# Kernel optimization log

Hardware: AMD Instinct MI355X
Metric: run time of the kernel (lower is better)

## Reference

```python
import jax, jax.numpy as jnp
import numpy as np

B, C, K, L = 2, 64, 256, 128
H = 8
DH = C // H
PROJ = 64
DADP = 10
FFT = 8
NG = 4
EPS = 1e-5
SCALE = float(1.0 / np.sqrt(DH))


def group_norm(x, g, b):
    # x: (B, C, N); GroupNorm(4, C)
    bb, cc, nn = x.shape
    xg = x.reshape(bb, NG, cc // NG, nn)
    mu = jnp.mean(xg, axis=(2, 3), keepdims=True)
    var = jnp.var(xg, axis=(2, 3), keepdims=True)
    xn = ((xg - mu) * jax.lax.rsqrt(var + EPS)).reshape(bb, cc, nn)
    return xn * g[None, :, None] + b[None, :, None]


def layer_norm(x, g, b):
    mu = jnp.mean(x, axis=-1, keepdims=True)
    var = jnp.var(x, axis=-1, keepdims=True)
    return (x - mu) * jax.lax.rsqrt(var + EPS) * g + b


def setup_inputs() -> dict:
    key = jax.random.key(0)
    ks = jax.random.split(key, 24)
    it = iter(ks)

    def nrm(shape, scale=0.05):
        return jax.random.normal(next(it), shape, dtype=jnp.float32) * scale

    z = lambda *s: jnp.zeros(s, jnp.float32)
    o = lambda *s: jnp.ones(s, jnp.float32)
    inp = dict(
        y=jax.random.normal(next(it), (B, C, K * L), dtype=jnp.float32),
        a1=jax.nn.softmax(jax.random.normal(next(it), (K, K), dtype=jnp.float32), axis=1),
        a2=jax.nn.softmax(jax.random.normal(next(it), (K, K), dtype=jnp.float32), axis=1),
        nodevec1=nrm((K, DADP), 0.3), nodevec2=nrm((DADP, K), 0.3),
        gcn_w=nrm((C, 7 * C)), gcn_b=z(C),
        s_wq=nrm((C, C)), s_wk=nrm((C, C)), s_wv=nrm((C, C)),
        s_pk=nrm((K, PROJ), float(1.0 / np.sqrt(PROJ))),
        s_pv=nrm((K, PROJ), float(1.0 / np.sqrt(PROJ))),
        s_wo=nrm((C, C)), s_bo=z(C),
        t_wq=nrm((C, C)), t_wk=nrm((C, C)), t_wv=nrm((C, C)),
        t_bq=z(C), t_bk=z(C), t_bv=z(C),
        t_wo=nrm((C, C)), t_bo=z(C),
        t_l1w=nrm((C, FFT)), t_l1b=z(FFT), t_l2w=nrm((FFT, C)), t_l2b=z(C),
        t_ln1g=o(C), t_ln1b=z(C), t_ln2g=o(C), t_ln2b=z(C),
        gn_local_g=o(C), gn_local_b=z(C),
        gn_s_g=o(C), gn_s_b=z(C),
        gn_t_g=o(C), gn_t_b=z(C),
        ff1_w=nrm((C, 2 * C)), ff1_b=z(2 * C),
        ff2_w=nrm((2 * C, C)), ff2_b=z(C),
        gn2_g=o(C), gn2_b=z(C),
        base_B=B, base_K=K, base_L=L,
    )
    return inp


def reference(y, a1, a2, nodevec1, nodevec2, gcn_w, gcn_b,
              s_wq, s_wk, s_wv, s_pk, s_pv, s_wo, s_bo,
              t_wq, t_wk, t_wv, t_bq, t_bk, t_bv, t_wo, t_bo,
              t_l1w, t_l1b, t_l2w, t_l2b, t_ln1g, t_ln1b, t_ln2g, t_ln2b,
              gn_local_g, gn_local_b, gn_s_g, gn_s_b, gn_t_g, gn_t_b,
              ff1_w, ff1_b, ff2_w, ff2_b, gn2_g, gn2_b,
              base_B, base_K, base_L):
    Bv, Kv, Lv = int(base_B), int(base_K), int(base_L)
    y4 = y.reshape(Bv, C, Kv, Lv)

    # ---- AdaptiveGCN: order-2 conv over [a1, a2, adaptive adj] + self ----
    x = y4.transpose(0, 3, 1, 2)  # (B, L, C, K)
    adp = jax.nn.softmax(jax.nn.relu(nodevec1 @ nodevec2), axis=1)  # (K, K)
    outs = [x]
    for a in (a1, a2, adp):
        x1 = jnp.einsum('blcv,wv->blcw', x, a)
        x2 = jnp.einsum('blcv,wv->blcw', x1, a)
        outs += [x1, x2]
    cat = jnp.concatenate(outs, axis=2)  # (B, L, 7C, K)
    g = jnp.einsum('blik,oi->blok', cat, gcn_w) + gcn_b[None, None, :, None]
    y_local = g.transpose(0, 2, 3, 1).reshape(Bv, C, Kv * Lv)
    y_local = group_norm(y + y_local, gn_local_g, gn_local_b)

    # ---- Linformer-style spatial attention over K ----
    xs = y4.transpose(0, 3, 2, 1).reshape(Bv * Lv, Kv, C)  # (B*L, K, C)
    q = (xs @ s_wq).reshape(-1, Kv, H, DH).transpose(0, 2, 1, 3)
    kp = jnp.einsum('bnd,nk->bkd', xs @ s_wk, s_pk).reshape(-1, PROJ, H, DH).transpose(0, 2, 1, 3)
    vp = jnp.einsum('bnd,nk->bkd', xs @ s_wv, s_pv).reshape(-1, PROJ, H, DH).transpose(0, 2, 1, 3)
    attn = jax.nn.softmax(jnp.einsum('bhnd,bhkd->bhnk', q, kp) * SCALE, axis=-1)
    o = jnp.einsum('bhnk,bhkd->bhnd', attn, vp).transpose(0, 2, 1, 3).reshape(-1, Kv, C)
    o = o @ s_wo + s_bo
    y_s = o.transpose(0, 2, 1).reshape(Bv, Lv, C, Kv).transpose(0, 2, 3, 1).reshape(Bv, C, Kv * Lv)
    y_s = group_norm(y + y_s, gn_s_g, gn_s_b)

    # ---- temporal transformer encoder layer over L ----
    xt = y4.transpose(0, 2, 3, 1).reshape(Bv * Kv, Lv, C)  # (B*K, L, C)
    tq = (xt @ t_wq + t_bq).reshape(-1, Lv, H, DH).transpose(0, 2, 1, 3)
    tk = (xt @ t_wk + t_bk).reshape(-1, Lv, H, DH).transpose(0, 2, 1, 3)
    tv = (xt @ t_wv + t_bv).reshape(-1, Lv, H, DH).transpose(0, 2, 1, 3)
    ta = jax.nn.softmax(jnp.einsum('bhnd,bhkd->bhnk', tq, tk) * SCALE, axis=-1)
    to = jnp.einsum('bhnk,bhkd->bhnd', ta, tv).transpose(0, 2, 1, 3).reshape(-1, Lv, C)
    to = to @ t_wo + t_bo
    src = layer_norm(xt + to, t_ln1g, t_ln1b)
    ff = jax.nn.gelu(src @ t_l1w + t_l1b, approximate=False) @ t_l2w + t_l2b
    src = layer_norm(src + ff, t_ln2g, t_ln2b)
    y_t = src.transpose(0, 2, 1).reshape(Bv, Kv, C, Lv).transpose(0, 2, 1, 3).reshape(Bv, C, Kv * Lv)
    y_t = group_norm(y + y_t, gn_t_g, gn_t_b)

    # ---- fuse + channel FFN + final norm ----
    y_in2 = y_local + y_s + y_t
    h = jax.nn.relu(y_in2.transpose(0, 2, 1) @ ff1_w + ff1_b)
    h = (h @ ff2_w + ff2_b).transpose(0, 2, 1)
    return group_norm(h + y_in2, gn2_g, gn2_b)
```

## Files before the change

### kernel.cpp

```cpp
#include <hip/hip_runtime.h>
#include <math.h>

constexpr int CC = 64, KK = 256, LL = 128;
constexpr int NN = KK * LL;
constexpr int PR = 64;
constexpr int CPG = 16;
constexpr float EPSV = 1e-5f;
constexpr float SCL = 0.35355339059327373f;

typedef __attribute__((ext_vector_type(8))) short short8;
typedef __attribute__((ext_vector_type(4))) float f32x4;

__device__ __forceinline__ unsigned short f2bf(float x) {
  union { float f; unsigned int u; } v; v.f = x;
  unsigned int r = (v.u + 0x7FFFu + ((v.u >> 16) & 1u)) >> 16;
  return (unsigned short)r;
}
__device__ __forceinline__ float bf2f(unsigned short x) {
  union { unsigned int u; float f; } v; v.u = ((unsigned int)x) << 16;
  return v.f;
}

__global__ __launch_bounds__(256) void k_adp(const float* __restrict__ nv1,
                                             const float* __restrict__ nv2,
// ... 291 lines not shown
      short8 b1 = *(const short8*)(wqT + (size_t)(ct * 16 + lr) * 64 + 32 + g * 8);
      acc[ct] = __builtin_amdgcn_mfma_f32_16x16x32_bf16(ax0, b0, acc[ct], 0, 0, 0);
      acc[ct] = __builtin_amdgcn_mfma_f32_16x16x32_bf16(ax1, b1, acc[ct], 0, 0, 0);
    }
#pragma unroll
    for (int ct = 0; ct < 4; ++ct)
#pragma unroll
      for (int reg = 0; reg < 4; ++reg)
        qb[(size_t)(r0 + w * 16 + g * 4 + reg) * 64 + ct * 16 + lr] = f2bf(acc[ct][reg]);
  }
  short8 bx0[4], bx1[4];
#pragma unroll
  for (int ct = 0; ct < 4; ++ct) {
    const unsigned short* bP = Xbf + (size_t)(r0 + ct * 16 + lr) * 64 + g * 8;
    bx0[ct] = *(const short8*)bP;
    bx1[ct] = *(const short8*)(bP + 32);
  }
  int bl = r0 >> 8, nb = r0 & 255;
#pragma unroll
  for (int which = 0; which < 2; ++which) {
    const unsigned short* WT = which ? wvT : wkT;
    unsigned short* dstb = which ? xvT : xkT;
    short8 aw0 = *(const short8*)(WT + (size_t)(w * 16 + lr) * 64 + g * 8);
    short8 aw1 = *(const short8*)(WT + (size_t)(w * 16 + lr) * 64 + 32 + g * 8);
    f32x4 acc[4];
#pragma unroll
    for (int ct = 0; ct < 4; ++ct) {
      acc[ct] = f32x4{0.f, 0.f, 0.f, 0.f};
      acc[ct] = __builtin_amdgcn_mfma_f32_16x16x32_bf16(aw0, bx0[ct], acc[ct], 0, 0, 0);
      acc[ct] = __builtin_amdgcn_mfma_f32_16x16x32_bf16(aw1, bx1[ct], acc[ct], 0, 0, 0);
    }
#pragma unroll
    for (int ct = 0; ct < 4; ++ct)
#pragma unroll
      for (int reg = 0; reg < 4; ++reg) {
        int o = w * 16 + g * 4 + reg;
        dstb[(size_t)bl * 16384 + (size_t)o * 256 + nb + ct * 16 + lr] = f2bf(acc[ct][reg]);
      }
  }
}

__global__ __launch_bounds__(256) void k_qkvt_M(const unsigned short* __restrict__ Xbf,
                                                const unsigned short* __restrict__ wqT,
                                                const unsigned short* __restrict__ wkT,
                                                const unsigned short* __restrict__ wvT,
                                                const float* __restrict__ bq, const float* __restrict__ bk_,
                                                const float* __restrict__ bv,
                                                unsigned short* __restrict__ qb,
                                                unsigned short* __restrict__ kb,
                                                unsigned short* __restrict__ vt) {
  int r0 = blockIdx.x * 64;
  int t = threadIdx.x, w = t >> 6, lane = t & 63;
  int lr = lane & 15, g = lane >> 4;
  const unsigned short* aP = Xbf + (size_t)(r0 + w * 16 + lr) * 64 + g * 8;
  short8 ax0 = *(const short8*)aP;
  short8 ax1 = *(const short8*)(aP + 32);
#pragma unroll
  for (int which = 0; which < 2; ++which) {
    const unsigned short* WT = which ? wkT : wqT;
    const float* bias = which ? bk_ : bq;
    unsigned short* dstb = which ? kb : qb;
    f32x4 acc[4];
#pragma unroll
    for (int ct = 0; ct < 4; ++ct) {
      acc[ct] = f32x4{0.f, 0.f, 0.f, 0.f};
      short8 b0 = *(const short8*)(WT + (size_t)(ct * 16 + lr) * 64 + g * 8);
      short8 b1 = *(const short8*)(WT + (size_t)(ct * 16 + lr) * 64 + 32 + g * 8);
      acc[ct] = __builtin_amdgcn_mfma_f32_16x16x32_bf16(ax0, b0, acc[ct], 0, 0, 0);
      acc[ct] = __builtin_amdgcn_mfma_f32_16x16x32_bf16(ax1, b1, acc[ct], 0, 0, 0);
    }
#pragma unroll
    for (int ct = 0; ct < 4; ++ct) {
      float bvv = bias[ct * 16 + lr];
#pragma unroll
      for (int reg = 0; reg < 4; ++reg)
        dstb[(size_t)(r0 + w * 16 + g * 4 + reg) * 64 + ct * 16 + lr] = f2bf(acc[ct][reg] + bvv);
    }
  }
  short8 bx0[4], bx1[4];
#pragma unroll
  for (int ct = 0; ct < 4; ++ct) {
    const unsigned short* bP = Xbf + (size_t)(r0 + ct * 16 + lr) * 64 + g * 8;
    bx0[ct] = *(const short8*)bP;
    bx1[ct] = *(const short8*)(bP + 32);
  }
  int bkk = r0 >> 7, lbase = r0 & 127;
  short8 aw0 = *(const short8*)(wvT + (size_t)(w * 16 + lr) * 64 + g * 8);
  short8 aw1 = *(const short8*)(wvT + (size_t)(w * 16 + lr) * 64 + 32 + g * 8);
  f32x4 acc[4];
#pragma unroll
  for (int ct = 0; ct < 4; ++ct) {
    acc[ct] = f32x4{0.f, 0.f, 0.f, 0.f};
    acc[ct] = __builtin_amdgcn_mfma_f32_16x16x32_bf16(aw0, bx0[ct], acc[ct], 0, 0, 0);
    acc[ct] = __builtin_amdgcn_mfma_f32_16x16x32_bf16(aw1, bx1[ct], acc[ct], 0, 0, 0);
  }
#pragma unroll
  for (int ct = 0; ct < 4; ++ct)
#pragma unroll
    for (int reg = 0; reg < 4; ++reg) {
      int o = w * 16 + g * 4 + reg;
      vt[(size_t)bkk * 8192 + (size_t)o * 128 + lbase + ct * 16 + lr] = f2bf(acc[ct][reg] + bv[o]);
    }
}

__global__ __launch_bounds__(256) void k_sprojM(const unsigned short* __restrict__ XkT,
                                                const unsigned short* __restrict__ XvT,
                                                const unsigned short* __restrict__ PkT,
                                                const unsigned short* __restrict__ PvT,
                                                unsigned short* __restrict__ kpb,
                                                unsigned short* __restrict__ vptb) {
  int bl = blockIdx.x;
  int which = blockIdx.y;
  int t = threadIdx.x, w = t >> 6, lane = t & 63;
  int lr = lane & 15, g = lane >> 4;
  const unsigned short* Abase = which ? PvT : XkT + (size_t)bl * 16384;
  const unsigned short* Bbase = which ? XvT + (size_t)bl * 16384 : PkT;
  const unsigned short* aP = Abase + (size_t)(w * 16 + lr) * 256 + g * 8;
  f32x4 acc[4];
#pragma unroll
  for (int ct = 0; ct < 4; ++ct) acc[ct] = f32x4{0.f, 0.f, 0.f, 0.f};
  for (int k0 = 0; k0 < 256; k0 += 32) {
    short8 af = *(const short8*)(aP + k0);
#pragma unroll
    for (int ct = 0; ct < 4; ++ct) {
      short8 bf = *(const short8*)(Bbase + (size_t)(ct * 16 + lr) * 256 + k0 + g * 8);
      acc[ct] = __builtin_amdgcn_mfma_f32_16x16x32_bf16(af, bf, acc[ct], 0, 0, 0);
    }
  }
  if (!which) {
    unsigned short* dst = kpb + (size_t)bl * 4096;
#pragma unroll
    for (int ct = 0; ct < 4; ++ct) {
      int p = ct * 16 + lr;
      int c0 = w * 16 + g * 4;
      ushort4 pk;
      pk.x = f2bf(acc[ct][0]); pk.y = f2bf(acc[ct][1]);
      pk.z = f2bf(acc[ct][2]); pk.w = f2bf(acc[ct][3]);
      *(ushort4*)&dst[(size_t)p * 64 + c0] = pk;
    }
  } else {
    unsigned short* dst = vptb + (size_t)bl * 4096;
#pragma unroll
    for (int ct = 0; ct < 4; ++ct) {
      int c = ct * 16 + lr;
      int p0 = w * 16 + g * 4;
      ushort4 pk;
      pk.x = f2bf(acc[ct][0]); pk.y = f2bf(acc[ct][1]);
      pk.z = f2bf(acc[ct][2]); pk.w = f2bf(acc[ct][3]);
      *(ushort4*)&dst[(size_t)c * 64 + p0] = pk;
    }
  }
}

__global__ __launch_bounds__(256) void k_lin64(const unsigned short* __restrict__ in,
                                               const unsigned short* __restrict__ WT,
                                               const float* __restrict__ bias,
                                               float* __restrict__ out) {
  int r0 = blockIdx.x * 64;
  int t = threadIdx.x, w = t >> 6, lane = t & 63;
  int lr = lane & 15, g = lane >> 4;
  const unsigned short* aP = in + (size_t)(r0 + w * 16 + lr) * 64 + g * 8;
  short8 af0 = *(const short8*)aP;
  short8 af1 = *(const short8*)(aP + 32);
  f32x4 acc[4];
#pragma unroll
  for (int ct = 0; ct < 4; ++ct) acc[ct] = f32x4{0.f, 0.f, 0.f, 0.f};
#pragma unroll
  for (int ct = 0; ct < 4; ++ct) {
    short8 b0 = *(const short8*)(WT + (size_t)(ct * 16 + lr) * 64 + g * 8);
    short8 b1 = *(const short8*)(WT + (size_t)(ct * 16 + lr) * 64 + 32 + g * 8);
    acc[ct] = __builtin_amdgcn_mfma_f32_16x16x32_bf16(af0, b0, acc[ct], 0, 0, 0);
    acc[ct] = __builtin_amdgcn_mfma_f32_16x16x32_bf16(af1, b1, acc[ct], 0, 0, 0);
  }
#pragma unroll
  for (int ct = 0; ct < 4; ++ct) {
    int o = ct * 16 + lr;
    float bv = bias[o];
#pragma unroll
    for (int reg = 0; reg < 4; ++reg)
      out[(size_t)(r0 + w * 16 + g * 4 + reg) * 64 + o] = acc[ct][reg] + bv;
  }
}

__global__ __launch_bounds__(256) void k_cffn(const unsigned short* __restrict__ in,
                                              const unsigned short* __restrict__ ff1T,
                                              const unsigned short* __restrict__ ff2T,
                                              const float* __restrict__ b1,
                                              const float* __restrict__ b2,
                                              float* __restrict__ out) {
  __shared__ unsigned short sH[4][16 * 128];
  int r0 = blockIdx.x * 64;
  int t = threadIdx.x, w = t >> 6, lane = t & 63;
  int lr = lane & 15, g = lane >> 4;
  unsigned short* myH = sH[w];
  const unsigned short* aP = in + (size_t)(r0 + w * 16 + lr) * 64 + g * 8;
  short8 af0 = *(const short8*)aP;
  short8 af1 = *(const short8*)(aP + 32);
  f32x4 acc1[8];
#pragma unroll
  for (int ct = 0; ct < 8; ++ct) acc1[ct] = f32x4{0.f, 0.f, 0.f, 0.f};
#pragma unroll
  for (int ct = 0; ct < 8; ++ct) {
    short8 b0 = *(const short8*)(ff1T + (size_t)(ct * 16 + lr) * 64 + g * 8);
    short8 bx = *(const short8*)(ff1T + (size_t)(ct * 16 + lr) * 64 + 32 + g * 8);
    acc1[ct] = __builtin_amdgcn_mfma_f32_16x16x32_bf16(af0, b0, acc1[ct], 0, 0, 0);
    acc1[ct] = __builtin_amdgcn_mfma_f32_16x16x32_bf16(af1, bx, acc1[ct], 0, 0, 0);
  }
#pragma unroll
  for (int ct = 0; ct < 8; ++ct) {
    int o = ct * 16 + lr;
    float bv = b1[o];
#pragma unroll
    for (int reg = 0; reg < 4; ++reg) {
      int m = g * 4 + reg;
      float h = fmaxf(acc1[ct][reg] + bv, 0.f);
      int bo = ((m * 128 + o) * 2) ^ ((m & 7) << 4);
      *(unsigned short*)((char*)myH + bo) = f2bf(h);
    }
  }
  __syncthreads();
  short8 ha[4];
#pragma unroll
  for (int ks = 0; ks < 4; ++ks) {
    int bo = ((lr * 128 + ks * 32 + g * 8) * 2) ^ ((lr & 7) << 4);
    ha[ks] = *(const short8*)((char*)myH + bo);
  }
  f32x4 acc2[4];
#pragma unroll
  for (int ct = 0; ct < 4; ++ct) acc2[ct] = f32x4{0.f, 0.f, 0.f, 0.f};
#pragma unroll
  for (int ct = 0; ct < 4; ++ct)
#pragma unroll
    for (int ks = 0; ks < 4; ++ks) {
      short8 b0 = *(const short8*)(ff2T + (size_t)(ct * 16 + lr) * 128 + ks * 32 + g * 8);
      acc2[ct] = __builtin_amdgcn_mfma_f32_16x16x32_bf16(ha[ks], b0, acc2[ct], 0, 0, 0);
    }
#pragma unroll
  for (int ct = 0; ct < 4; ++ct) {
    int o = ct * 16 + lr;
    float bv = b2[o];
#pragma unroll
    for (int reg = 0; reg < 4; ++reg)
      out[(size_t)(r0 + w * 16 + g * 4 + reg) * 64 + o] = acc2[ct][reg] + bv;
  }
}

__global__ __launch_bounds__(256) void k_tffn(const float* __restrict__ A, const float* __restrict__ Bz,
                                              const float* __restrict__ l1w, const float* __restrict__ l1b,
                                              const float* __restrict__ l2w, const float* __restrict__ l2b,
                                              const float* __restrict__ ln1g, const float* __restrict__ ln1b,
                                              const float* __restrict__ ln2g, const float* __restrict__ ln2b,
                                              float* __restrict__ outp) {
  int r0 = blockIdx.x * 64;
  __shared__ float sSrc[64][65];
  __shared__ float sH[64][8];
  __shared__ float sW1[64][8];
  __shared__ float sW2[8][64];
  int t = threadIdx.x;
  for (int i = t; i < 512; i += 256) { ((float*)sW1)[i] = l1w[i]; ((float*)sW2)[i] = l2w[i]; }
  int c = t & 63, rg = t >> 6;
  float g1 = ln1g[c], be1 = ln1b[c];
  for (int it = 0; it < 16; ++it) {
    int r = it * 4 + rg;
    size_t idx = (size_t)(r0 + r) * 64 + c;
    float x = A[idx] + Bz[idx];
    float s = x, ss = x * x;
#pragma unroll
    for (int off = 32; off; off >>= 1) { s += __shfl_xor(s, off); ss += __shfl_xor(ss, off); }
    float mu = s * (1.f / 64.f);
    float var = ss * (1.f / 64.f) - mu * mu;
    sSrc[r][c] = (x - mu) * rsqrtf(var + EPSV) * g1 + be1;
  }
  __syncthreads();
#pragma unroll
  for (int p = 0; p < 2; ++p) {
    int idx = t + 256 * p;
    int row = idx >> 3, j = idx & 7;
    float acc = l1b[j];
    for (int cc = 0; cc < 64; ++cc) acc += sSrc[row][cc] * sW1[cc][j];
    acc = 0.5f * acc * (1.f + erff(acc * 0.70710678118654752440f));
    sH[row][j] = acc;
  }
  __syncthreads();
  float g2 = ln2g[c], be2 = ln2b[c];
  float l2bc = l2b[c];
  for (int it = 0; it < 16; ++it) {
    int r = it * 4 + rg;
    float o = l2bc;
#pragma unroll
    for (int j = 0; j < 8; ++j) o += sH[r][j] * sW2[j][c];
    float x = sSrc[r][c] + o;
    float s = x, ss = x * x;
#pragma unroll
    for (int off = 32; off; off >>= 1) { s += __shfl_xor(s, off); ss += __shfl_xor(ss, off); }
    float mu = s * (1.f / 64.f);
    float var = ss * (1.f / 64.f) - mu * mu;
    outp[(size_t)(r0 + r) * 64 + c] = (x - mu) * rsqrtf(var + EPSV) * g2 + be2;
  }
}

template <int NKV, int KVSHIFT>
__global__ __launch_bounds__(512) void k_attnH(const unsigned short* __restrict__ Qb,
                                               const unsigned short* __restrict__ Kb,
                                               const unsigned short* __restrict__ VTb,
                                               unsigned short* __restrict__ O) {
  constexpr int NCT = NKV / 16;
  constexpr int NKS = NKV / 32;
  int blk = blockIdx.x;
  const unsigned short* Qp = Qb + (size_t)blk * 128 * 64;
  unsigned short* Op = O + (size_t)blk * 128 * 64;
  const unsigned short* Kp = Kb + (size_t)(blk >> KVSHIFT) * NKV * 64;
  const unsigned short* VTp = VTb + (size_t)(blk >> KVSHIFT) * 64 * NKV;
  int t = threadIdx.x;
  int h = t >> 6, lane = t & 63, lr = lane & 15, g = lane >> 4;
  __shared__ unsigned short sP[8][16 * NKV];
  unsigned short* myP = sP[h];

  short8 kbf[NCT];
#pragma unroll
  for (int ct = 0; ct < NCT; ++ct)
    kbf[ct] = *(const short8*)(Kp + (size_t)(ct * 16 + lr) * 64 + h * 8);

  int vr = h * 8 + lr; if (vr > 63) vr = 63;
  short8 vbf[NKS];
#pragma unroll
  for (int ks = 0; ks < NKS; ++ks)
    vbf[ks] = *(const short8*)(VTp + (size_t)vr * NKV + ks * 32 + g * 8);

  for (int mt = 0; mt < 8; ++mt) {
    short8 qa = short8{0, 0, 0, 0, 0, 0, 0, 0};
    if (g == 0) qa = *(const short8*)(Qp + (size_t)(mt * 16 + lr) * 64 + h * 8);

    f32x4 sacc[NCT];
#pragma unroll
    for (int ct = 0; ct < NCT; ++ct) sacc[ct] = f32x4{0.f, 0.f, 0.f, 0.f};
#pragma unroll
    for (int ct = 0; ct < NCT; ++ct)
      sacc[ct] = __builtin_amdgcn_mfma_f32_16x16x32_bf16(qa, kbf[ct], sacc[ct], 0, 0, 0);

    float inv4[4];
#pragma unroll
    for (int reg = 0; reg < 4; ++reg) {
      float s = 0.f;
#pragma unroll
      for (int ct = 0; ct < NCT; ++ct) {
        float e = __expf(sacc[ct][reg] * SCL);
        sacc[ct][reg] = e;
        s += e;
      }
      s += __shfl_xor(s, 1); s += __shfl_xor(s, 2); s += __shfl_xor(s, 4); s += __shfl_xor(s, 8);
      inv4[reg] = 1.f / s;
    }

#pragma unroll
    for (int ct = 0; ct < NCT; ++ct)
#pragma unroll
      for (int reg = 0; reg < 4; ++reg) {
        int row = g * 4 + reg;
        int bo = ((row * NKV + ct * 16 + lr) * 2) ^ ((row & 7) << 4);
        *(unsigned short*)((char*)myP + bo) = f2bf(sacc[ct][reg]);
      }
    __syncthreads();

    f32x4 oacc = f32x4{0.f, 0.f, 0.f, 0.f};
#pragma unroll
    for (int ks = 0; ks < NKS; ++ks) {
      int bo = ((lr * NKV + ks * 32 + g * 8) * 2) ^ ((lr & 7) << 4);
      short8 pa = *(const short8*)((char*)myP + bo);
      oacc = __builtin_amdgcn_mfma_f32_16x16x32_bf16(pa, vbf[ks], oacc, 0, 0, 0);
    }
    if (lr < 8) {
#pragma unroll
      for (int reg = 0; reg < 4; ++reg) {
        int row = mt * 16 + g * 4 + reg;
        Op[(size_t)row * 64 + h * 8 + lr] = f2bf(oacc[reg] * inv4[reg]);
      }
    }
    __syncthreads();
  }
}

__global__ __launch_bounds__(256) void k_gn_part(const float* __restrict__ p0, const float* __restrict__ p1,
                                                 const float* __restrict__ p2, const float* __restrict__ p3,
                                                 const float* __restrict__ p4,
                                                 float* __restrict__ sumOut,
                                                 float* __restrict__ part) {
  int bg = blockIdx.y, blk = blockIdx.x, t = threadIdx.x;
  size_t start = (size_t)bg * ((size_t)CPG * NN) + (size_t)blk * 8192;
  const float4* q0 = (const float4*)(p0 + start);
  const float4* q1 = p1 ? (const float4*)(p1 + start) : nullptr;
  const float4* q2 = p2 ? (const float4*)(p2 + start) : nullptr;
  const float4* q3 = p3 ? (const float4*)(p3 + start) : nullptr;
  const float4* q4 = p4 ? (const float4*)(p4 + start) : nullptr;
  float4* so = sumOut ? (float4*)(sumOut + start) : nullptr;
  float s = 0.f, ss = 0.f;
  for (int i = t; i < 2048; i += 256) {
    float4 x = q0[i];
    if (q1) { float4 y4 = q1[i]; x.x += y4.x; x.y += y4.y; x.z += y4.z; x.w += y4.w; }
    if (q2) { float4 y4 = q2[i]; x.x += y4.x; x.y += y4.y; x.z += y4.z; x.w += y4.w; }
    if (q3) { float4 y4 = q3[i]; x.x += y4.x; x.y += y4.y; x.z += y4.z; x.w += y4.w; }
    if (q4) { float4 y4 = q4[i]; x.x += y4.x; x.y += y4.y; x.z += y4.z; x.w += y4.w; }
    if (so) so[i] = x;
    s += x.x + x.y + x.z + x.w;
    ss += x.x * x.x + x.y * x.y + x.z * x.z + x.w * x.w;
  }
  __shared__ float rs[256], rq[256];
  rs[t] = s; rq[t] = ss; __syncthreads();
  for (int off = 128; off; off >>= 1) { if (t < off) { rs[t] += rs[t + off]; rq[t] += rq[t + off]; } __syncthreads(); }
  if (t == 0) { part[(bg * 64 + blk) * 2] = rs[0]; part[(bg * 64 + blk) * 2 + 1] = rq[0]; }
}

__global__ __launch_bounds__(256) void k_gn_partB(const float* __restrict__ p0,
                                                  const unsigned short* __restrict__ q1,
                                                  const unsigned short* __restrict__ q2,
                                                  const unsigned short* __restrict__ q3,
                                                  const unsigned short* __restrict__ q4,
                                                  float* __restrict__ sumOut,
                                                  float* __restrict__ part) {
  int bg = blockIdx.y, blk = blockIdx.x, t = threadIdx.x;
  size_t start = (size_t)bg * ((size_t)CPG * NN) + (size_t)blk * 8192;
  const float4* f0 = (const float4*)(p0 + start);
  const ushort4* b1 = (const ushort4*)(q1 + start);
  const ushort4* b2 = (const ushort4*)(q2 + start);
  const ushort4* b3 = (const ushort4*)(q3 + start);
  const ushort4* b4 = (const ushort4*)(q4 + start);
  float4* so = (float4*)(sumOut + start);
  float s = 0.f, ss = 0.f;
  for (int i = t; i < 2048; i += 256) {
    float4 x = f0[i];
    ushort4 u;
    u = b1[i]; x.x += bf2f(u.x); x.y += bf2f(u.y); x.z += bf2f(u.z); x.w += bf2f(u.w);
    u = b2[i]; x.x += bf2f(u.x); x.y += bf2f(u.y); x.z += bf2f(u.z); x.w += bf2f(u.w);
    u = b3[i]; x.x += bf2f(u.x); x.y += bf2f(u.y); x.z += bf2f(u.z); x.w += bf2f(u.w);
    u = b4[i]; x.x += bf2f(u.x); x.y += bf2f(u.y); x.z += bf2f(u.z); x.w += bf2f(u.w);
    so[i] = x;
    s += x.x + x.y + x.z + x.w;
    ss += x.x * x.x + x.y * x.y + x.z * x.z + x.w * x.w;
  }
  __shared__ float rs[256], rq[256];
  rs[t] = s; rq[t] = ss; __syncthreads();
  for (int off = 128; off; off >>= 1) { if (t < off) { rs[t] += rs[t + off]; rq[t] += rq[t + off]; } __syncthreads(); }
  if (t == 0) { part[(bg * 64 + blk) * 2] = rs[0]; part[(bg * 64 + blk) * 2 + 1] = rq[0]; }
}

__global__ __launch_bounds__(256) void k_gn_apply(const float* __restrict__ p0, const float* __restrict__ p1,
                                                  const float* __restrict__ part, const float* __restrict__ g,
                                                  const float* __restrict__ be,
                                                  const float* __restrict__ q0, const float* __restrict__ q1,
                                                  float* __restrict__ out) {
  size_t i4 = (size_t)blockIdx.x * 256 + threadIdx.x;
  size_t i = i4 * 4;
  int chan = (int)(i >> 15) & 63;
  int bg = (int)(i >> 19);
  __shared__ float smu, srr;
  int t = threadIdx.x;
  if (t < 64) {
    float s = part[(bg * 64 + t) * 2], ss = part[(bg * 64 + t) * 2 + 1];
#pragma unroll
    for (int off = 32; off; off >>= 1) { s += __shfl_xor(s, off); ss += __shfl_xor(ss, off); }
    if (t == 0) {
      float inv = 1.f / (float)((size_t)CPG * NN);
      float mu = s * inv;
      float var = ss * inv - mu * mu;
      smu = mu; srr = rsqrtf(var + EPSV);
    }
  }
  __syncthreads();
  float mu = smu, rr = srr;
  float4 x = ((const float4*)p0)[i4];
  if (p1) { float4 y4 = ((const float4*)p1)[i4]; x.x += y4.x; x.y += y4.y; x.z += y4.z; x.w += y4.w; }
  float gc = g[chan], bc = be[chan];
  float4 v;
  v.x = (x.x - mu) * rr * gc + bc;
  v.y = (x.y - mu) * rr * gc + bc;
  v.z = (x.z - mu) * rr * gc + bc;
  v.w = (x.w - mu) * rr * gc + bc;
  if (q0) { float4 y4 = ((const float4*)q0)[i4]; v.x += y4.x; v.y += y4.y; v.z += y4.z; v.w += y4.w; }
  if (q1) { float4 y4 = ((const float4*)q1)[i4]; v.x += y4.x; v.y += y4.y; v.z += y4.z; v.w += y4.w; }
  ((float4*)out)[i4] = v;
}

__global__ __launch_bounds__(256) void k_gn_apply3(const float* __restrict__ SL, const float* __restrict__ SS,
                                                   const float* __restrict__ ST,
                                                   const float* __restrict__ part,
                                                   const float* __restrict__ gl, const float* __restrict__ bl_,
                                                   const float* __restrict__ gs, const float* __restrict__ bs_,
                                                   const float* __restrict__ gt, const float* __restrict__ bt_,
                                                   float* __restrict__ out) {
  size_t i4 = (size_t)blockIdx.x * 256 + threadIdx.x;
  size_t i = i4 * 4;
  int chan = (int)(i >> 15) & 63;
  int bg = (int)(i >> 19);
  __shared__ float smu[3], srr[3];
  int t = threadIdx.x;
  if (t < 192) {
    int which = t >> 6, tt = t & 63;
    const float* pp = part + which * 2048;
    float s = pp[(bg * 64 + tt) * 2], ss = pp[(bg * 64 + tt) * 2 + 1];
#pragma unroll
    for (int off = 32; off; off >>= 1) { s += __shfl_xor(s, off); ss += __shfl_xor(ss, off); }
    if (tt == 0) {
      float inv = 1.f / (float)((size_t)CPG * NN);
      float mu = s * inv;
      float var = ss * inv - mu * mu;
      smu[which] = mu; srr[which] = rsqrtf(var + EPSV);
    }
  }
  __syncthreads();
  float mL = smu[0], rL = srr[0];
  float mS = smu[1], rS = srr[1];
  float mT = smu[2], rT = srr[2];
  float gL = gl[chan] * rL, bL = bl_[chan] - mL * gl[chan] * rL;
  float gS = gs[chan] * rS, bS = bs_[chan] - mS * gs[chan] * rS;
  float gT = gt[chan] * rT, bT = bt_[chan] - mT * gt[chan] * rT;
  float4 xl = ((const float4*)SL)[i4];
  float4 xs = ((const float4*)SS)[i4];
  float4 xt = ((const float4*)ST)[i4];
  float4 v;
  v.x = xl.x * gL + bL + xs.x * gS + bS + xt.x * gT + bT;
  v.y = xl.y * gL + bL + xs.y * gS + bS + xt.y * gT + bT;
  v.z = xl.z * gL + bL + xs.z * gS + bS + xt.z * gT + bT;
  v.w = xl.w * gL + bL + xs.w * gS + bS + xt.w * gT + bT;
  ((float4*)out)[i4] = v;
}

extern "C" void kernel_launch(void* const* d_in, const int* in_sizes, int n_in,
                              void* d_out, int out_size, void* d_ws, size_t ws_size,
                              hipStream_t stream) {
  (void)in_sizes; (void)n_in; (void)out_size; (void)ws_size;
  const float* y     = (const float*)d_in[0];
  const float* a1    = (const float*)d_in[1];
  const float* a2    = (const float*)d_in[2];
  const float* nv1   = (const float*)d_in[3];
  const float* nv2   = (const float*)d_in[4];
  const float* gcn_w = (const float*)d_in[5];
  const float* gcn_b = (const float*)d_in[6];
  const float* s_wq  = (const float*)d_in[7];
  const float* s_wk  = (const float*)d_in[8];
  const float* s_wv  = (const float*)d_in[9];
  const float* s_pk  = (const float*)d_in[10];
  const float* s_pv  = (const float*)d_in[11];
  const float* s_wo  = (const float*)d_in[12];
  const float* s_bo  = (const float*)d_in[13];
  const float* t_wq  = (const float*)d_in[14];
  const float* t_wk  = (const float*)d_in[15];
  const float* t_wv  = (const float*)d_in[16];
  const float* t_bq  = (const float*)d_in[17];
  const float* t_bk  = (const float*)d_in[18];
  const float* t_bv  = (const float*)d_in[19];
  const float* t_wo  = (const float*)d_in[20];
  const float* t_bo  = (const float*)d_in[21];
  const float* t_l1w = (const float*)d_in[22];
  const float* t_l1b = (const float*)d_in[23];
  const float* t_l2w = (const float*)d_in[24];
  const float* t_l2b = (const float*)d_in[25];
  const float* ln1g  = (const float*)d_in[26];
  const float* ln1b  = (const float*)d_in[27];
  const float* ln2g  = (const float*)d_in[28];
  const float* ln2b  = (const float*)d_in[29];
  const float* gnlg  = (const float*)d_in[30];
  const float* gnlb  = (const float*)d_in[31];
  const float* gnsg  = (const float*)d_in[32];
  const float* gnsb  = (const float*)d_in[33];
  const float* gntg  = (const float*)d_in[34];
  const float* gntb  = (const float*)d_in[35];
  const float* ff1w  = (const float*)d_in[36];
  const float* ff1b  = (const float*)d_in[37];
  const float* ff2w  = (const float*)d_in[38];
  const float* ff2b  = (const float*)d_in[39];
  const float* gn2g  = (const float*)d_in[40];
  const float* gn2b  = (const float*)d_in[41];

  float* ws = (float*)d_ws;
  float* part  = ws + 65536;
  unsigned short* a1_bf   = (unsigned short*)(ws + 131072);
  unsigned short* a2_bf   = (unsigned short*)(ws + 163840);
  unsigned short* adp_bf  = (unsigned short*)(ws + 196608);
  unsigned short* gcnw_bf = (unsigned short*)(ws + 229376);
  unsigned short* xs_bf   = (unsigned short*)(ws + 262144);
  unsigned short* swoT = (unsigned short*)(ws + 2359296);
  unsigned short* twoT = (unsigned short*)(ws + 2361344);
  unsigned short* ff1T = (unsigned short*)(ws + 2363392);
  unsigned short* ff2T = (unsigned short*)(ws + 2367488);
  unsigned short* swqT = (unsigned short*)(ws + 2371584);
  unsigned short* swkT = (unsigned short*)(ws + 2373632);
  unsigned short* swvT = (unsigned short*)(ws + 2375680);
  unsigned short* twqT = (unsigned short*)(ws + 2377728);
  unsigned short* twkT = (unsigned short*)(ws + 2379776);
  unsigned short* twvT = (unsigned short*)(ws + 2381824);
  unsigned short* PkT  = (unsigned short*)(ws + 2383872);
  unsigned short* PvT  = (unsigned short*)(ws + 2392064);
  unsigned short* kpb  = (unsigned short*)(ws + 131072);
  unsigned short* vptb = (unsigned short*)(ws + 1179648);
  const size_t SLOT = 4194304;
  float* G0 = ws + SLOT * 1;
  float* G1 = ws + SLOT * 2;
  float* G2 = ws + SLOT * 3;
  float* G3 = ws + SLOT * 4;
  float* G4 = ws + SLOT * 5;
  float* G5 = ws + SLOT * 6;
  float* G6 = ws + SLOT * 7;
  unsigned short* U1 = (unsigned short*)G3;
  unsigned short* U2 = (unsigned short*)G3 + 4194304;
  unsigned short* U3 = (unsigned short*)G4;
  unsigned short* U4 = (unsigned short*)G4 + 4194304;
  unsigned short* U5 = (unsigned short*)G5;
  unsigned short* U6 = (unsigned short*)G5 + 4194304;
  unsigned short* s0bf = (unsigned short*)G1;
  unsigned short* Q1bf = (unsigned short*)G0;
  unsigned short* Q3bf = (unsigned short*)G0 + 4194304;
  unsigned short* Q2bf = (unsigned short*)G6;
  unsigned short* qbuf = (unsigned short*)G0;
  unsigned short* xkT = (unsigned short*)G4;
  unsigned short* xvT = (unsigned short*)G5;
  unsigned short* kbuf = (unsigned short*)G4;
  unsigned short* vtbuf = (unsigned short*)G5;
  unsigned short* xt_bf = (unsigned short*)G6;
  float* out = (float*)d_out;

  const long BS = 2097152;

  k_adp<<<256, 256, 0, stream>>>(nv1, nv2, adp_bf);
  k_castW<<<960, 256, 0, stream>>>(a1, a2, gcn_w, s_wo, t_wo, ff1w, ff2w,
                                   s_wq, s_wk, s_wv, t_wq, t_wk, t_wv, s_pk, s_pv,
                                   a1_bf, a2_bf, gcnw_bf, swoT, twoT, ff1T, ff2T,
                                   swqT, swkT, swvT, twqT, twkT, twvT, PkT, PvT);

  k_tr<<<dim3(512, 8), 256, 0, stream>>>(y, nullptr, nullptr, xs_bf, BS, 128, 32768, 1, BS, 64, 1, 16384, 64, 128);

  k_mix0<<<1024, 64, 0, stream>>>(xs_bf, gcnw_bf, gcn_b, s0bf);
  k_mix6<<<dim3(1024, 3), 64, 0, stream>>>(xs_bf, gcnw_bf, U1, U2, U3, U4, U5, U6);
  k_adj2M<<<512, 256, 0, stream>>>(a1_bf, U2, U1, Q1bf);
  k_adj2M<<<512, 256, 0, stream>>>(a2_bf, U4, U3, Q2bf);
  k_adj2M<<<512, 256, 0, stream>>>(adp_bf, U6, U5, Q3bf);
  k_gn_partB<<<dim3(64, 8), 256, 0, stream>>>(y, s0bf, Q1bf, Q2bf, Q3bf, G3, part);

  k_qkvs_M<<<1024, 256, 0, stream>>>(xs_bf, swqT, swkT, swvT, qbuf, xkT, xvT);
  k_sprojM<<<dim3(256, 2), 256, 0, stream>>>(xkT, xvT, PkT, PvT, kpb, vptb);
  k_attnH<64, 1><<<512, 512, 0, stream>>>(qbuf, kpb, vptb, (unsigned short*)G6);
  k_lin64<<<1024, 256, 0, stream>>>((unsigned short*)G6, swoT, s_bo, G4);
  k_tr<<<dim3(512, 8), 256, 0, stream>>>(G4, G1, y, nullptr, BS, 64, 16384, 1, BS, 128, 1, 32768, 128, 64);
  k_gn_part<<<dim3(64, 8), 256, 0, stream>>>(G1, nullptr, nullptr, nullptr, nullptr, nullptr, part + 2048);

  k_tr<<<dim3(512, 8), 256, 0, stream>>>(y, G2, nullptr, xt_bf, BS, 128, 32768, 1, BS, 8192, 1, 64, 64, 128);
  k_qkvt_M<<<1024, 256, 0, stream>>>(xt_bf, twqT, twkT, twvT, t_bq, t_bk, t_bv, qbuf, kbuf, vtbuf);
  k_attnH<128, 0><<<512, 512, 0, stream>>>(qbuf, kbuf, vtbuf, (unsigned short*)G6);
  k_lin64<<<1024, 256, 0, stream>>>((unsigned short*)G6, twoT, t_bo, G4);
  k_tffn<<<1024, 256, 0, stream>>>(G2, G4, t_l1w, t_l1b, t_l2w, t_l2b,
                                   ln1g, ln1b, ln2g, ln2b, G6);
  k_tr<<<dim3(512, 8), 256, 0, stream>>>(G6, G2, y, nullptr, BS, 8192, 64, 1, BS, 128, 1, 32768, 128, 64);
  k_gn_part<<<dim3(64, 8), 256, 0, stream>>>(G2, nullptr, nullptr, nullptr, nullptr, nullptr, part + 4096);

  k_gn_apply3<<<4096, 256, 0, stream>>>(G3, G1, G2, part, gnlg, gnlb, gnsg, gnsb, gntg, gntb, G3);

  k_tr<<<dim3(512, 8), 256, 0, stream>>>(G3, nullptr, nullptr, (unsigned short*)G4,
                                         BS, 128, 32768, 1, BS, 8192, 1, 64, 64, 128);
  k_cffn<<<1024, 256, 0, stream>>>((unsigned short*)G4, ff1T, ff2T, ff1b, ff2b, G5);
  k_tr<<<dim3(512, 8), 256, 0, stream>>>(G5, out, G3, nullptr, BS, 8192, 64, 1, BS, 128, 1, 32768, 128, 64);
  k_gn_part<<<dim3(64, 8), 256, 0, stream>>>(out, nullptr, nullptr, nullptr, nullptr, nullptr, part);
  k_gn_apply<<<4096, 256, 0, stream>>>(out, nullptr, part, gn2g, gn2b, nullptr, nullptr, out);
}
```

Measured before the change: 366.3 us.

## Fuse attention output projection into attention kernels and store branch sums in bf16

The attention kernels now stage their per-head outputs in swizzled shared memory and apply the 64x64 output projection plus bias themselves, which removes the separate k_lin64 launches and the bf16 round trip through global memory. The local, spatial and temporal residual sums are now written as bf16 instead of fp32, and new bf16 variants of the group-norm partial and apply kernels read them. This roughly halves the memory traffic for those intermediates at the cost of extra bf16 rounding before normalization. It also adds 16 KB of shared memory per attention block, which may reduce occupancy.

Result: no change. 359.4 us (-1.9%).

```diff
diff --git a/kernel.cpp b/kernel.cpp
--- a/kernel.cpp
+++ b/kernel.cpp
@@ -467,36 +467,6 @@
   }
 }
 
-__global__ __launch_bounds__(256) void k_lin64(const unsigned short* __restrict__ in,
-                                               const unsigned short* __restrict__ WT,
-                                               const float* __restrict__ bias,
-                                               float* __restrict__ out) {
-  int r0 = blockIdx.x * 64;
-  int t = threadIdx.x, w = t >> 6, lane = t & 63;
-  int lr = lane & 15, g = lane >> 4;
-  const unsigned short* aP = in + (size_t)(r0 + w * 16 + lr) * 64 + g * 8;
-  short8 af0 = *(const short8*)aP;
-  short8 af1 = *(const short8*)(aP + 32);
-  f32x4 acc[4];
-#pragma unroll
-  for (int ct = 0; ct < 4; ++ct) acc[ct] = f32x4{0.f, 0.f, 0.f, 0.f};
-#pragma unroll
-  for (int ct = 0; ct < 4; ++ct) {
-    short8 b0 = *(const short8*)(WT + (size_t)(ct * 16 + lr) * 64 + g * 8);
-    short8 b1 = *(const short8*)(WT + (size_t)(ct * 16 + lr) * 64 + 32 + g * 8);
-    acc[ct] = __builtin_amdgcn_mfma_f32_16x16x32_bf16(af0, b0, acc[ct], 0, 0, 0);
-    acc[ct] = __builtin_amdgcn_mfma_f32_16x16x32_bf16(af1, b1, acc[ct], 0, 0, 0);
-  }
-#pragma unroll
-  for (int ct = 0; ct < 4; ++ct) {
-    int o = ct * 16 + lr;
-    float bv = bias[o];
-#pragma unroll
-    for (int reg = 0; reg < 4; ++reg)
-      out[(size_t)(r0 + w * 16 + g * 4 + reg) * 64 + o] = acc[ct][reg] + bv;
-  }
-}
-
 __global__ __launch_bounds__(256) void k_cffn(const unsigned short* __restrict__ in,
                                               const unsigned short* __restrict__ ff1T,
                                               const unsigned short* __restrict__ ff2T,
@@ -615,20 +585,22 @@
 }
 
 template <int NKV, int KVSHIFT>
-__global__ __launch_bounds__(512) void k_attnH(const unsigned short* __restrict__ Qb,
+__global__ __launch_bounds__(512) void k_attnP(const unsigned short* __restrict__ Qb,
                                                const unsigned short* __restrict__ Kb,
                                                const unsigned short* __restrict__ VTb,
-                                               unsigned short* __restrict__ O) {
+                                               const unsigned short* __restrict__ WT,
+                                               const float* __restrict__ bias,
+                                               float* __restrict__ out) {
   constexpr int NCT = NKV / 16;
   constexpr int NKS = NKV / 32;
   int blk = blockIdx.x;
   const unsigned short* Qp = Qb + (size_t)blk * 128 * 64;
-  unsigned short* Op = O + (size_t)blk * 128 * 64;
   const unsigned short* Kp = Kb + (size_t)(blk >> KVSHIFT) * NKV * 64;
   const unsigned short* VTp = VTb + (size_t)(blk >> KVSHIFT) * 64 * NKV;
   int t = threadIdx.x;
   int h = t >> 6, lane = t & 63, lr = lane & 15, g = lane >> 4;
   __shared__ unsigned short sP[8][16 * NKV];
+  __shared__ unsigned short sO[128 * 64];
   unsigned short* myP = sP[h];
 
   short8 kbf[NCT];
@@ -688,36 +660,68 @@
 #pragma unroll
       for (int reg = 0; reg < 4; ++reg) {
         int row = mt * 16 + g * 4 + reg;
-        Op[(size_t)row * 64 + h * 8 + lr] = f2bf(oacc[reg] * inv4[reg]);
+        int col = h * 8 + lr;
+        int bo = ((row * 64 + col) * 2) ^ ((row & 7) << 4);
+        *(unsigned short*)((char*)sO + bo) = f2bf(oacc[reg] * inv4[reg]);
       }
     }
     __syncthreads();
   }
-}
-
-__global__ __launch_bounds__(256) void k_gn_part(const float* __restrict__ p0, const float* __restrict__ p1,
-                                                 const float* __restrict__ p2, const float* __restrict__ p3,
-                                                 const float* __restrict__ p4,
-                                                 float* __restrict__ sumOut,
+
+  int row = h * 16 + lr;
+  int bo0 = ((row * 64 + g * 8) * 2) ^ ((row & 7) << 4);
+  int bo1 = ((row * 64 + 32 + g * 8) * 2) ^ ((row & 7) << 4);
+  short8 af0 = *(const short8*)((char*)sO + bo0);
+  short8 af1 = *(const short8*)((char*)sO + bo1);
+  f32x4 acc[4];
+#pragma unroll
+  for (int ct = 0; ct < 4; ++ct) acc[ct] = f32x4{0.f, 0.f, 0.f, 0.f};
+#pragma unroll
+  for (int ct = 0; ct < 4; ++ct) {
+    short8 b0 = *(const short8*)(WT + (size_t)(ct * 16 + lr) * 64 + g * 8);
+    short8 b1 = *(const short8*)(WT + (size_t)(ct * 16 + lr) * 64 + 32 + g * 8);
+    acc[ct] = __builtin_amdgcn_mfma_f32_16x16x32_bf16(af0, b0, acc[ct], 0, 0, 0);
+    acc[ct] = __builtin_amdgcn_mfma_f32_16x16x32_bf16(af1, b1, acc[ct], 0, 0, 0);
+  }
+  float* op = out + (size_t)blk * 128 * 64;
+#pragma unroll
+  for (int ct = 0; ct < 4; ++ct) {
+    int o = ct * 16 + lr;
+    float bv = bias[o];
+#pragma unroll
+    for (int reg = 0; reg < 4; ++reg)
+      op[(size_t)(h * 16 + g * 4 + reg) * 64 + o] = acc[ct][reg] + bv;
+  }
+}
+
+__global__ __launch_bounds__(256) void k_gn_part(const float* __restrict__ p0,
                                                  float* __restrict__ part) {
   int bg = blockIdx.y, blk = blockIdx.x, t = threadIdx.x;
   size_t start = (size_t)bg * ((size_t)CPG * NN) + (size_t)blk * 8192;
   const float4* q0 = (const float4*)(p0 + start);
-  const float4* q1 = p1 ? (const float4*)(p1 + start) : nullptr;
-  const float4* q2 = p2 ? (const float4*)(p2 + start) : nullptr;
-  const float4* q3 = p3 ? (const float4*)(p3 + start) : nullptr;
-  const float4* q4 = p4 ? (const float4*)(p4 + start) : nullptr;
-  float4* so = sumOut ? (float4*)(sumOut + start) : nullptr;
   float s = 0.f, ss = 0.f;
   for (int i = t; i < 2048; i += 256) {
     float4 x = q0[i];
-    if (q1) { float4 y4 = q1[i]; x.x += y4.x; x.y += y4.y; x.z += y4.z; x.w += y4.w; }
-    if (q2) { float4 y4 = q2[i]; x.x += y4.x; x.y += y4.y; x.z += y4.z; x.w += y4.w; }
-    if (q3) { float4 y4 = q3[i]; x.x += y4.x; x.y += y4.y; x.z += y4.z; x.w += y4.w; }
-    if (q4) { float4 y4 = q4[i]; x.x += y4.x; x.y += y4.y; x.z += y4.z; x.w += y4.w; }
-    if (so) so[i] = x;
     s += x.x + x.y + x.z + x.w;
     ss += x.x * x.x + x.y * x.y + x.z * x.z + x.w * x.w;
+  }
+  __shared__ float rs[256], rq[256];
+  rs[t] = s; rq[t] = ss; __syncthreads();
+  for (int off = 128; off; off >>= 1) { if (t < off) { rs[t] += rs[t + off]; rq[t] += rq[t + off]; } __syncthreads(); }
+  if (t == 0) { part[(bg * 64 + blk) * 2] = rs[0]; part[(bg * 64 + blk) * 2 + 1] = rq[0]; }
+}
+
+__global__ __launch_bounds__(256) void k_gn_part1B(const unsigned short* __restrict__ p0,
+                                                   float* __restrict__ part) {
+  int bg = blockIdx.y, blk = blockIdx.x, t = threadIdx.x;
+  size_t start = (size_t)bg * ((size_t)CPG * NN) + (size_t)blk * 8192;
+  const ushort4* q0 = (const ushort4*)(p0 + start);
+  float s = 0.f, ss = 0.f;
+  for (int i = t; i < 2048; i += 256) {
+    ushort4 u = q0[i];
+    float a = bf2f(u.x), b = bf2f(u.y), c = bf2f(u.z), d = bf2f(u.w);
+    s += a + b + c + d;
+    ss += a * a + b * b + c * c + d * d;
   }
   __shared__ float rs[256], rq[256];
   rs[t] = s; rq[t] = ss; __syncthreads();
@@ -730,7 +734,7 @@
                                                   const unsigned short* __restrict__ q2,
                                                   const unsigned short* __restrict__ q3,
                                                   const unsigned short* __restrict__ q4,
-                                                  float* __restrict__ sumOut,
+                                                  unsigned short* __restrict__ sumOut,
                                                   float* __restrict__ part) {
   int bg = blockIdx.y, blk = blockIdx.x, t = threadIdx.x;
   size_t start = (size_t)bg * ((size_t)CPG * NN) + (size_t)blk * 8192;
@@ -739,7 +743,7 @@
   const ushort4* b2 = (const ushort4*)(q2 + start);
   const ushort4* b3 = (const ushort4*)(q3 + start);
   const ushort4* b4 = (const ushort4*)(q4 + start);
-  float4* so = (float4*)(sumOut + start);
+  ushort4* so = (ushort4*)(sumOut + start);
   float s = 0.f, ss = 0.f;
   for (int i = t; i < 2048; i += 256) {
     float4 x = f0[i];
@@ -748,7 +752,9 @@
     u = b2[i]; x.x += bf2f(u.x); x.y += bf2f(u.y); x.z += bf2f(u.z); x.w += bf2f(u.w);
     u = b3[i]; x.x += bf2f(u.x); x.y += bf2f(u.y); x.z += bf2f(u.z); x.w += bf2f(u.w);
     u = b4[i]; x.x += bf2f(u.x); x.y += bf2f(u.y); x.z += bf2f(u.z); x.w += bf2f(u.w);
-    so[i] = x;
+    ushort4 pk;
+    pk.x = f2bf(x.x); pk.y = f2bf(x.y); pk.z = f2bf(x.z); pk.w = f2bf(x.w);
+    so[i] = pk;
     s += x.x + x.y + x.z + x.w;
     ss += x.x * x.x + x.y * x.y + x.z * x.z + x.w * x.w;
   }
@@ -758,10 +764,9 @@
   if (t == 0) { part[(bg * 64 + blk) * 2] = rs[0]; part[(bg * 64 + blk) * 2 + 1] = rq[0]; }
 }
 
-__global__ __launch_bounds__(256) void k_gn_apply(const float* __restrict__ p0, const float* __restrict__ p1,
+__global__ __launch_bounds__(256) void k_gn_apply(const float* __restrict__ p0,
                                                   const float* __restrict__ part, const float* __restrict__ g,
                                                   const float* __restrict__ be,
-                                                  const float* __restrict__ q0, const float* __restrict__ q1,
                                                   float* __restrict__ out) {
   size_t i4 = (size_t)blockIdx.x * 256 + threadIdx.x;
   size_t i = i4 * 4;
@@ -783,25 +788,23 @@
   __syncthreads();
   float mu = smu, rr = srr;
   float4 x = ((const float4*)p0)[i4];
-  if (p1) { float4 y4 = ((const float4*)p1)[i4]; x.x += y4.x; x.y += y4.y; x.z += y4.z; x.w += y4.w; }
   float gc = g[chan], bc = be[chan];
   float4 v;
   v.x = (x.x - mu) * rr * gc + bc;
   v.y = (x.y - mu) * rr * gc + bc;
   v.z = (x.z - mu) * rr * gc + bc;
   v.w = (x.w - mu) * rr * gc + bc;
-  if (q0) { float4 y4 = ((const float4*)q0)[i4]; v.x += y4.x; v.y += y4.y; v.z += y4.z; v.w += y4.w; }
-  if (q1) { float4 y4 = ((const float4*)q1)[i4]; v.x += y4.x; v.y += y4.y; v.z += y4.z; v.w += y4.w; }
   ((float4*)out)[i4] = v;
 }
 
-__global__ __launch_bounds__(256) void k_gn_apply3(const float* __restrict__ SL, const float* __restrict__ SS,
-                                                   const float* __restrict__ ST,
-                                                   const float* __restrict__ part,
-                                                   const float* __restrict__ gl, const float* __restrict__ bl_,
-                                                   const float* __restrict__ gs, const float* __restrict__ bs_,
-                                                   const float* __restrict__ gt, const float* __restrict__ bt_,
-                                                   float* __restrict__ out) {
+__global__ __launch_bounds__(256) void k_gn_apply3B(const unsigned short* __restrict__ SLb,
+                                                    const unsigned short* __restrict__ SSb,
+                                                    const unsigned short* __restrict__ STb,
+                                                    const float* __restrict__ part,
+                                                    const float* __restrict__ gl, const float* __restrict__ bl_,
+                                                    const float* __restrict__ gs, const float* __restrict__ bs_,
+                                                    const float* __restrict__ gt, const float* __restrict__ bt_,
+                                                    float* __restrict__ out) {
   size_t i4 = (size_t)blockIdx.x * 256 + threadIdx.x;
   size_t i = i4 * 4;
   int chan = (int)(i >> 15) & 63;
@@ -822,20 +825,17 @@
     }
   }
   __syncthreads();
-  float mL = smu[0], rL = srr[0];
-  float mS = smu[1], rS = srr[1];
-  float mT = smu[2], rT = srr[2];
-  float gL = gl[chan] * rL, bL = bl_[chan] - mL * gl[chan] * rL;
-  float gS = gs[chan] * rS, bS = bs_[chan] - mS * gs[chan] * rS;
-  float gT = gt[chan] * rT, bT = bt_[chan] - mT * gt[chan] * rT;
-  float4 xl = ((const float4*)SL)[i4];
-  float4 xs = ((const float4*)SS)[i4];
-  float4 xt = ((const float4*)ST)[i4];
+  float gL = gl[chan] * srr[0], bL = bl_[chan] - smu[0] * gl[chan] * srr[0];
+  float gS = gs[chan] * srr[1], bS = bs_[chan] - smu[1] * gs[chan] * srr[1];
+  float gT = gt[chan] * srr[2], bT = bt_[chan] - smu[2] * gt[chan] * srr[2];
+  ushort4 ul = ((const ushort4*)SLb)[i4];
+  ushort4 us = ((const ushort4*)SSb)[i4];
+  ushort4 ut = ((const ushort4*)STb)[i4];
   float4 v;
-  v.x = xl.x * gL + bL + xs.x * gS + bS + xt.x * gT + bT;
-  v.y = xl.y * gL + bL + xs.y * gS + bS + xt.y * gT + bT;
-  v.z = xl.z * gL + bL + xs.z * gS + bS + xt.z * gT + bT;
-  v.w = xl.w * gL + bL + xs.w * gS + bS + xt.w * gT + bT;
+  v.x = bf2f(ul.x) * gL + bL + bf2f(us.x) * gS + bS + bf2f(ut.x) * gT + bT;
+  v.y = bf2f(ul.y) * gL + bL + bf2f(us.y) * gS + bS + bf2f(ut.y) * gT + bT;
+  v.z = bf2f(ul.z) * gL + bL + bf2f(us.z) * gS + bS + bf2f(ut.z) * gT + bT;
+  v.w = bf2f(ul.w) * gL + bL + bf2f(us.w) * gS + bS + bf2f(ut.w) * gT + bT;
   ((float4*)out)[i4] = v;
 }
 
@@ -925,6 +925,9 @@
   unsigned short* Q1bf = (unsigned short*)G0;
   unsigned short* Q3bf = (unsigned short*)G0 + 4194304;
   unsigned short* Q2bf = (unsigned short*)G6;
+  unsigned short* SLb  = (unsigned short*)G3;
+  unsigned short* SSb  = (unsigned short*)G1;
+  unsigned short* STb  = (unsigned short*)G2;
   unsigned short* qbuf = (unsigned short*)G0;
   unsigned short* xkT = (unsigned short*)G4;
   unsigned short* xvT = (unsigned short*)G5;
@@ -948,30 +951,28 @@
   k_adj2M<<<512, 256, 0, stream>>>(a1_bf, U2, U1, Q1bf);
   k_adj2M<<<512, 256, 0, stream>>>(a2_bf, U4, U3, Q2bf);
   k_adj2M<<<512, 256, 0, stream>>>(adp_bf, U6, U5, Q3bf);
-  k_gn_partB<<<dim3(64, 8), 256, 0, stream>>>(y, s0bf, Q1bf, Q2bf, Q3bf, G3, part);
+  k_gn_partB<<<dim3(64, 8), 256, 0, stream>>>(y, s0bf, Q1bf, Q2bf, Q3bf, SLb, part);
 
   k_qkvs_M<<<1024, 256, 0, stream>>>(xs_bf, swqT, swkT, swvT, qbuf, xkT, xvT);
   k_sprojM<<<dim3(256, 2), 256, 0, stream>>>(xkT, xvT, PkT, PvT, kpb, vptb);
-  k_attnH<64, 1><<<512, 512, 0, stream>>>(qbuf, kpb, vptb, (unsigned short*)G6);
-  k_lin64<<<1024, 256, 0, stream>>>((unsigned short*)G6, swoT, s_bo, G4);
-  k_tr<<<dim3(512, 8), 256, 0, stream>>>(G4, G1, y, nullptr, BS, 64, 16384, 1, BS, 128, 1, 32768, 128, 64);
-  k_gn_part<<<dim3(64, 8), 256, 0, stream>>>(G1, nullptr, nullptr, nullptr, nullptr, nullptr, part + 2048);
+  k_attnP<64, 1><<<512, 512, 0, stream>>>(qbuf, kpb, vptb, swoT, s_bo, G4);
+  k_tr<<<dim3(512, 8), 256, 0, stream>>>(G4, nullptr, y, SSb, BS, 64, 16384, 1, BS, 128, 1, 32768, 128, 64);
+  k_gn_part1B<<<dim3(64, 8), 256, 0, stream>>>(SSb, part + 2048);
 
   k_tr<<<dim3(512, 8), 256, 0, stream>>>(y, G2, nullptr, xt_bf, BS, 128, 32768, 1, BS, 8192, 1, 64, 64, 128);
   k_qkvt_M<<<1024, 256, 0, stream>>>(xt_bf, twqT, twkT, twvT, t_bq, t_bk, t_bv, qbuf, kbuf, vtbuf);
-  k_attnH<128, 0><<<512, 512, 0, stream>>>(qbuf, kbuf, vtbuf, (unsigned short*)G6);
-  k_lin64<<<1024, 256, 0, stream>>>((unsigned short*)G6, twoT, t_bo, G4);
-  k_tffn<<<1024, 256, 0, stream>>>(G2, G4, t_l1w, t_l1b, t_l2w, t_l2b,
-                                   ln1g, ln1b, ln2g, ln2b, G6);
-  k_tr<<<dim3(512, 8), 256, 0, stream>>>(G6, G2, y, nullptr, BS, 8192, 64, 1, BS, 128, 1, 32768, 128, 64);
-  k_gn_part<<<dim3(64, 8), 256, 0, stream>>>(G2, nullptr, nullptr, nullptr, nullptr, nullptr, part + 4096);
-
-  k_gn_apply3<<<4096, 256, 0, stream>>>(G3, G1, G2, part, gnlg, gnlb, gnsg, gnsb, gntg, gntb, G3);
-
-  k_tr<<<dim3(512, 8), 256, 0, stream>>>(G3, nullptr, nullptr, (unsigned short*)G4,
+  k_attnP<128, 0><<<512, 512, 0, stream>>>(qbuf, kbuf, vtbuf, twoT, t_bo, G6);
+  k_tffn<<<1024, 256, 0, stream>>>(G2, G6, t_l1w, t_l1b, t_l2w, t_l2b,
+                                   ln1g, ln1b, ln2g, ln2b, G0);
+  k_tr<<<dim3(512, 8), 256, 0, stream>>>(G0, nullptr, y, STb, BS, 8192, 64, 1, BS, 128, 1, 32768, 128, 64);
+  k_gn_part1B<<<dim3(64, 8), 256, 0, stream>>>(STb, part + 4096);
+
+  k_gn_apply3B<<<4096, 256, 0, stream>>>(SLb, SSb, STb, part, gnlg, gnlb, gnsg, gnsb, gntg, gntb, G4);
+
+  k_tr<<<dim3(512, 8), 256, 0, stream>>>(G4, nullptr, nullptr, (unsigned short*)G5,
                                          BS, 128, 32768, 1, BS, 8192, 1, 64, 64, 128);
-  k_cffn<<<1024, 256, 0, stream>>>((unsigned short*)G4, ff1T, ff2T, ff1b, ff2b, G5);
-  k_tr<<<dim3(512, 8), 256, 0, stream>>>(G5, out, G3, nullptr, BS, 8192, 64, 1, BS, 128, 1, 32768, 128, 64);
-  k_gn_part<<<dim3(64, 8), 256, 0, stream>>>(out, nullptr, nullptr, nullptr, nullptr, nullptr, part);
-  k_gn_apply<<<4096, 256, 0, stream>>>(out, nullptr, part, gn2g, gn2b, nullptr, nullptr, out);
-}
+  k_cffn<<<1024, 256, 0, stream>>>((unsigned short*)G5, ff1T, ff2T, ff1b, ff2b, G6);
+  k_tr<<<dim3(512, 8), 256, 0, stream>>>(G6, out, G4, nullptr, BS, 8192, 64, 1, BS, 128, 1, 32768, 128, 64);
+  k_gn_part<<<dim3(64, 8), 256, 0, stream>>>(out, part);
+  k_gn_apply<<<4096, 256, 0, stream>>>(out, part, gn2g, gn2b, out);
+}
```
